# Performance work log

Hardware: AMD Instinct MI355X
Metric: run time of the kernel (lower is better)

Reference implementation:

```python
import jax, jax.numpy as jnp
import numpy as np

EPS = 1e-5

def _rmsnorm(x, eps=1e-6):
    # non-affine RMSNorm over last dim (BitNet SubLN-style pre-quant norm)
    return x * jax.lax.rsqrt(jnp.mean(x * x, axis=-1, keepdims=True) + eps)

def _act_quant(x):
    # per-token int8 absmax quantization
    scale = 127.0 / jnp.clip(jnp.max(jnp.abs(x), axis=-1, keepdims=True), EPS)
    return jnp.clip(jnp.round(x * scale), -128, 127) / scale

def _weight_quant(w):
    # per-tensor ternary (1.58-bit) quantization
    scale = 1.0 / jnp.clip(jnp.mean(jnp.abs(w)), EPS)
    return jnp.clip(jnp.round(w * scale), -1, 1) / scale

def _ste(a, q):
    # straight-through estimator: forward = q, backward grad flows to a
    return a + jax.lax.stop_gradient(q - a)

def _bitlinear(x, w):
    # x: [..., in_features], w: [out_features, in_features], no bias
    xn = _rmsnorm(x)
    xq = _ste(xn, _act_quant(xn))
    wq = _ste(w, _weight_quant(w))
    return jnp.einsum('bsd,hd->bsh', xq, wq)


def setup_inputs() -> dict:
    key = jax.random.key(0)
    k_x, k1, k2, k3 = jax.random.split(key, 4)
    B, S, D, H = 4, 4096, 2048, 5632  # hidden = 256*ceil(2048*8/3 / 256)
    return {
        'x': jax.random.normal(k_x, (B, S, D), dtype=jnp.float32),
        'w1': jax.random.normal(k1, (H, D), dtype=jnp.float32) * 0.02,
        'w2': jax.random.normal(k2, (H, D), dtype=jnp.float32) * 0.02,
        'w3': jax.random.normal(k3, (D, H), dtype=jnp.float32) * 0.02,
    }


def reference(x, w1, w2, w3):
    gate = jax.nn.silu(_bitlinear(x, w1))
    up = _bitlinear(x, w2)
    return _bitlinear(gate * up, w3)
```

## Files before the change

kernel.cpp:

```cpp
#include <hip/hip_runtime.h>

typedef int i32x4 __attribute__((ext_vector_type(4)));

static constexpr int M_TOK = 16384;
static constexpr int D_IN  = 2048;
static constexpr int H_FF  = 5632;
static constexpr int NW    = H_FF * D_IN;

__device__ __forceinline__ void async16(const void* g, void* l) {
    __builtin_amdgcn_global_load_lds((__attribute__((address_space(1))) void*)g,
                                     (__attribute__((address_space(3))) void*)l,
                                     16, 0, 0);
}

__device__ __forceinline__ void sbar() {
    asm volatile("" ::: "memory");
    __builtin_amdgcn_s_barrier();
    asm volatile("" ::: "memory");
}
#define WAIT_LGKM(n) { asm volatile("s_waitcnt lgkmcnt(" #n ")" ::: "memory"); \
                       __builtin_amdgcn_sched_barrier(0); }
#define WAIT_VM(n)   { asm volatile("s_waitcnt vmcnt(" #n ")" ::: "memory"); }

__global__ void absum_partial(const float4* __restrict__ w, int n4, double* __restrict__ part) {
    __shared__ double s[256];
    const int t = threadIdx.x;
    double acc = 0.0;
    for (int i = blockIdx.x * 256 + t; i < n4; i += gridDim.x * 256) {
        float4 v = w[i];
        acc += fabs((double)v.x) + fabs((double)v.y) + fabs((double)v.z) + fabs((double)v.w);
    }
    s[t] = acc;
    __syncthreads();
    for (int o = 128; o > 0; o >>= 1) {
        if (t < o) s[t] += s[t + o];
        __syncthreads();
    }
    if (t == 0) part[blockIdx.x] = s[0];
}

__global__ void finalize_scales(const double* __restrict__ parts, double* __restrict__ scales,
                                int nblocks, double inv_n) {
    const int t = threadIdx.x;
    if (t < 3) {
        const double* p = parts + t * nblocks;
        double s = 0.0;
        for (int i = 0; i < nblocks; ++i) s += p[i];
        double c = fmax(s * inv_n, 1e-5);
        scales[t * 2]     = 1.0 / c;
        scales[t * 2 + 1] = c;
    }
}

__global__ void quant_w_kernel(const float4* __restrict__ w, unsigned int* __restrict__ tw,
                               const double* __restrict__ scales, int idx, int n4) {
    const double s = scales[idx * 2];
    const int stride = gridDim.x * blockDim.x;
    for (int i = blockIdx.x * blockDim.x + threadIdx.x; i < n4; i += stride) {
        float4 v = w[i];
        int q0 = (int)fmin(fmax(rint((double)v.x * s), -1.0), 1.0);
        int q1 = (int)fmin(fmax(rint((double)v.y * s), -1.0), 1.0);
        int q2 = (int)fmin(fmax(rint((double)v.z * s), -1.0), 1.0);
        int q3 = (int)fmin(fmax(rint((double)v.w * s), -1.0), 1.0);
        tw[i] = (unsigned int)((q0 & 255) | ((q1 & 255) << 8) |
                               ((q2 & 255) << 16) | ((q3 & 255) << 24));
    }
}

__global__ void quant_x_kernel(const float* __restrict__ x, signed char* __restrict__ qx,
                               double* __restrict__ cx) {
    __shared__ double ssum[256];
    __shared__ float  smax[256];
    const int token = blockIdx.x;
    const int t = threadIdx.x;
    const float4* xr = (const float4*)(x + (size_t)token * D_IN);
    float4 v0 = xr[t];
    float4 v1 = xr[t + 256];
    double ss = (double)v0.x*v0.x + (double)v0.y*v0.y + (double)v0.z*v0.z + (double)v0.w*v0.w
              + (double)v1.x*v1.x + (double)v1.y*v1.y + (double)v1.z*v1.z + (double)v1.w*v1.w;
    float mx = fmaxf(fmaxf(fmaxf(fabsf(v0.x), fabsf(v0.y)), fmaxf(fabsf(v0.z), fabsf(v0.w))),
                     fmaxf(fmaxf(fabsf(v1.x), fabsf(v1.y)), fmaxf(fabsf(v1.z), fabsf(v1.w))));
    ssum[t] = ss; smax[t] = mx;
    __syncthreads();
    for (int o = 128; o > 0; o >>= 1) {
        if (t < o) { ssum[t] += ssum[t + o]; smax[t] = fmaxf(smax[t], smax[t + o]); }
        __syncthreads();
    }
    const double ms    = ssum[0] * (1.0 / (double)D_IN);
    const double r     = 1.0 / sqrt(ms + 1e-6);
    const double den   = fmax((double)smax[0] * r, 1e-5);
    const double scale = 127.0 / den;
    if (t == 0) cx[token] = den * (1.0 / 127.0);

    int q0 = (int)fmin(fmax(rint(((double)v0.x * r) * scale), -128.0), 127.0);
    int q1 = (int)fmin(fmax(rint(((double)v0.y * r) * scale), -128.0), 127.0);
    int q2 = (int)fmin(fmax(rint(((double)v0.z * r) * scale), -128.0), 127.0);
    int q3 = (int)fmin(fmax(rint(((double)v0.w * r) * scale), -128.0), 127.0);
    int q4 = (int)fmin(fmax(rint(((double)v1.x * r) * scale), -128.0), 127.0);
    int q5 = (int)fmin(fmax(rint(((double)v1.y * r) * scale), -128.0), 127.0);
    int q6 = (int)fmin(fmax(rint(((double)v1.z * r) * scale), -128.0), 127.0);
    int q7 = (int)fmin(fmax(rint(((double)v1.w * r) * scale), -128.0), 127.0);
    unsigned int* qr = (unsigned int*)(qx + (size_t)token * D_IN);
    qr[t]       = (unsigned int)((q0 & 255) | ((q1 & 255) << 8) | ((q2 & 255) << 16) | ((q3 & 255) << 24));
    qr[t + 256] = (unsigned int)((q4 & 255) | ((q5 & 255) << 8) | ((q6 & 255) << 16) | ((q7 & 255) << 24));
}

__global__ void quant_h_kernel(float* __restrict__ h, double* __restrict__ ch) {
    __shared__ double ssum[256];
    __shared__ float  smax[256];
    const int token = blockIdx.x;
    const int t = threadIdx.x;
    float* hr = h + (size_t)token * H_FF;
    const float2* h2 = (const float2*)hr;
    float2 vals[11];
    double ss = 0.0;
    float mx = 0.f;
#pragma unroll
    for (int k = 0; k < 11; ++k) {
        float2 v = h2[t + 256 * k];
        vals[k] = v;
        ss += (double)v.x * (double)v.x + (double)v.y * (double)v.y;
        mx = fmaxf(mx, fmaxf(fabsf(v.x), fabsf(v.y)));
    }
    ssum[t] = ss; smax[t] = mx;
    __syncthreads();
    for (int o = 128; o > 0; o >>= 1) {
        if (t < o) { ssum[t] += ssum[t + o]; smax[t] = fmaxf(smax[t], smax[t + o]); }
        __syncthreads();
    }
    const double ms    = ssum[0] * (1.0 / (double)H_FF);
    const double r     = 1.0 / sqrt(ms + 1e-6);
    const double den   = fmax((double)smax[0] * r, 1e-5);
    const double scale = 127.0 / den;
    if (t == 0) ch[token] = den * (1.0 / 127.0);
    unsigned short* qr = (unsigned short*)hr;
#pragma unroll
    for (int k = 0; k < 11; ++k) {
        int a = (int)fmin(fmax(rint(((double)vals[k].x * r) * scale), -128.0), 127.0);
        int b = (int)fmin(fmax(rint(((double)vals[k].y * r) * scale), -128.0), 127.0);
        qr[t + 256 * k] = (unsigned short)((a & 255) | ((b & 255) << 8));
    }
}


__global__ void __launch_bounds__(512, 4) gemm12_kernel(
    const signed char* __restrict__ qx,
    const signed char* __restrict__ tw1,
    const double* __restrict__ cx,
    const double* __restrict__ scales,
    float* __restrict__ h)
{
    __shared__ __attribute__((aligned(16))) signed char lds[2][24576];

    const int t = threadIdx.x;
    const int swz = (blockIdx.x & 7) * 704 + (blockIdx.x >> 3);
    const int bm  = swz / 88;
    const int bn  = swz % 88;

    const int srow = t >> 2;
    const int scol = (((t & 3) ^ ((t >> 3) & 3)) << 4);
    const signed char* gA = qx + (size_t)(bm * 256 + srow) * D_IN + scol;
    const size_t arstep = (size_t)128 * D_IN;
    const int brow = srow & 63;
    const signed char* gB = tw1 + (srow >= 64 ? (size_t)NW : (size_t)0)
                                + (size_t)(bn * 64 + brow) * D_IN + scol;
    const int l16 = t * 16;

    const int lane = t & 63;
    const int wv = t >> 6;
    const int wm = wv & 3;
    const int wn = wv >> 2;
    const int lm = lane & 15;
    const int kg = lane >> 4;
    const int koff  = ((kg ^ ((lm >> 1) & 3)) << 4);
    const int abase = (wm * 64 + lm) * 64 + koff;
    const int bbase = 16384 + (wn * 32 + lm) * 64 + koff;

    const i32x4 izero = {0, 0, 0, 0};
    i32x4 acc1[4][2], acc2[4][2];
#pragma unroll
    for (int i = 0; i < 4; ++i)
#pragma unroll
        for (int j = 0; j < 2; ++j) { acc1[i][j] = izero; acc2[i][j] = izero; }

    constexpr int NT = D_IN / 64;

#define STAGE12(buf, kt) { const int go = (kt) * 64;                         \
        async16(gA + go,          &lds[buf][l16]);                           \
        async16(gA + arstep + go, &lds[buf][8192 + l16]);                    \
        async16(gB + go,          &lds[buf][16384 + l16]); }

    STAGE12(0, 0);
    WAIT_VM(0); sbar();

    for (int kt = 0; kt < NT; ++kt) {
        const int cur = kt & 1;
        if (kt + 1 < NT) STAGE12(cur ^ 1, kt + 1);

        i32x4 a[4], b1[2], b2[2];
#pragma unroll
        for (int i = 0; i < 4; ++i) a[i] = *(const i32x4*)&lds[cur][abase + i * 1024];
#pragma unroll
        for (int j = 0; j < 2; ++j) b1[j] = *(const i32x4*)&lds[cur][bbase + j * 1024];
        __builtin_amdgcn_sched_barrier(0);
#pragma unroll
        for (int j = 0; j < 2; ++j) b2[j] = *(const i32x4*)&lds[cur][bbase + 4096 + j * 1024];

        WAIT_LGKM(2);
        __builtin_amdgcn_s_setprio(1);
#pragma unroll
        for (int i = 0; i < 4; ++i)
#pragma unroll
            for (int j = 0; j < 2; ++j)
                acc1[i][j] = __builtin_amdgcn_mfma_i32_16x16x64_i8(a[i], b1[j], acc1[i][j], 0, 0, 0);
        __builtin_amdgcn_s_setprio(0);
        WAIT_LGKM(0);
        __builtin_amdgcn_s_setprio(1);
#pragma unroll
        for (int i = 0; i < 4; ++i)
#pragma unroll
            for (int j = 0; j < 2; ++j)
                acc2[i][j] = __builtin_amdgcn_mfma_i32_16x16x64_i8(a[i], b2[j], acc2[i][j], 0, 0, 0);
        __builtin_amdgcn_s_setprio(0);

        WAIT_VM(0);
        sbar();
    }
#undef STAGE12

    const double cw1 = scales[1];
    const double cw2 = scales[3];
#pragma unroll
    for (int i = 0; i < 4; ++i) {
#pragma unroll
        for (int v = 0; v < 4; ++v) {
            const int row = bm * 256 + wm * 64 + i * 16 + kg * 4 + v;
            const double c  = cx[row];
            const double s1 = c * cw1, s2 = c * cw2;
            float* hp = h + (size_t)row * H_FF + bn * 64 + wn * 32 + lm;
#pragma unroll
            for (int j = 0; j < 2; ++j) {
                float g  = (float)((double)acc1[i][j][v] * s1);
                float u  = (float)((double)acc2[i][j][v] * s2);
                float sg = g / (1.0f + expf(-g));
                hp[j * 16] = sg * u;
            }
        }
    }
}

__global__ void __launch_bounds__(512, 4) gemm3_kernel(
    const signed char* __restrict__ qh,
    const signed char* __restrict__ tw3,
    const double* __restrict__ ch,
    const double* __restrict__ scales,
    float* __restrict__ out)
{
    __shared__ __attribute__((aligned(16))) signed char lds[2][24576];

    const int t = threadIdx.x;
    const int swz = (blockIdx.x & 7) * 128 + (blockIdx.x >> 3);
    const int bm  = swz >> 4;
    const int bn  = swz & 15;

    const int srow = t >> 2;
    const int scol = (((t & 3) ^ ((t >> 3) & 3)) << 4);
    const size_t qh_stride = (size_t)4 * H_FF;
    const signed char* gA = qh  + (size_t)(bm * 256 + srow) * qh_stride + scol;
    const signed char* gB = tw3 + (size_t)(bn * 128 + srow) * H_FF + scol;
    const size_t arstep = (size_t)128 * qh_stride;
    const int l16 = t * 16;

    const int lane = t & 63;
    const int wv = t >> 6;
    const int wm = wv & 3;
    const int wn = wv >> 2;
    const int lm = lane & 15;
    const int kg = lane >> 4;
    const int koff  = ((kg ^ ((lm >> 1) & 3)) << 4);
    const int abase = (wm * 64 + lm) * 64 + koff;
    const int bbase = 16384 + (wn * 64 + lm) * 64 + koff;

    const i32x4 izero = {0, 0, 0, 0};
    i32x4 acc[4][4];
#pragma unroll
    for (int i = 0; i < 4; ++i)
#pragma unroll
        for (int j = 0; j < 4; ++j) acc[i][j] = izero;

    constexpr int NT = H_FF / 64;

#define STAGE3(buf, kt) { const int go = (kt) * 64;                          \
        async16(gA + go,          &lds[buf][l16]);                           \
        async16(gA + arstep + go, &lds[buf][8192 + l16]);                    \
        async16(gB + go,          &lds[buf][16384 + l16]); }

    STAGE3(0, 0);
    WAIT_VM(0); sbar();

    for (int kt = 0; kt < NT; ++kt) {
        const int cur = kt & 1;
        if (kt + 1 < NT) STAGE3(cur ^ 1, kt + 1);

        i32x4 a[4], b[4];
#pragma unroll
        for (int i = 0; i < 4; ++i) a[i] = *(const i32x4*)&lds[cur][abase + i * 1024];
#pragma unroll
        for (int j = 0; j < 2; ++j) b[j] = *(const i32x4*)&lds[cur][bbase + j * 1024];
        __builtin_amdgcn_sched_barrier(0);
#pragma unroll
        for (int j = 2; j < 4; ++j) b[j] = *(const i32x4*)&lds[cur][bbase + j * 1024];

        WAIT_LGKM(2);
        __builtin_amdgcn_s_setprio(1);
#pragma unroll
        for (int i = 0; i < 4; ++i)
#pragma unroll
            for (int j = 0; j < 2; ++j)
                acc[i][j] = __builtin_amdgcn_mfma_i32_16x16x64_i8(a[i], b[j], acc[i][j], 0, 0, 0);
        __builtin_amdgcn_s_setprio(0);
        WAIT_LGKM(0);
        __builtin_amdgcn_s_setprio(1);
#pragma unroll
        for (int i = 0; i < 4; ++i)
#pragma unroll
            for (int j = 2; j < 4; ++j)
                acc[i][j] = __builtin_amdgcn_mfma_i32_16x16x64_i8(a[i], b[j], acc[i][j], 0, 0, 0);
        __builtin_amdgcn_s_setprio(0);

        WAIT_VM(0);
        sbar();
    }
#undef STAGE3

    const double cw3 = scales[5];
#pragma unroll
    for (int i = 0; i < 4; ++i) {
#pragma unroll
        for (int v = 0; v < 4; ++v) {
            const int row = bm * 256 + wm * 64 + i * 16 + kg * 4 + v;
            const double sc = ch[row] * cw3;
            float* op = out + (size_t)row * D_IN + bn * 128 + wn * 64 + lm;
#pragma unroll
            for (int j = 0; j < 4; ++j) op[j * 16] = (float)((double)acc[i][j][v] * sc);
        }
    }
}

extern "C" void kernel_launch(void* const* d_in, const int* in_sizes, int n_in,
                              void* d_out, int out_size, void* d_ws, size_t ws_size,
                              hipStream_t stream) {
    const float* x  = (const float*)d_in[0];
    const float* w1 = (const float*)d_in[1];
    const float* w2 = (const float*)d_in[2];
    const float* w3 = (const float*)d_in[3];

    char* ws = (char*)d_ws;
    double*      scales = (double*)(ws + 0);
    double*      parts  = (double*)(ws + 256);
    double*      cx     = (double*)(ws + 25088);
    double*      ch     = (double*)(ws + 156416);
    signed char* tw1    = (signed char*)(ws + 287744);
    signed char* tw2    = (signed char*)(ws + 11822080);
    signed char* tw3    = (signed char*)(ws + 23356416);
    float*       hb     = (float*)(ws + 34891520);
    signed char* qx     = (signed char*)(ws + 403990528);

    absum_partial<<<1024, 256, 0, stream>>>((const float4*)w1, NW / 4, parts);
    absum_partial<<<1024, 256, 0, stream>>>((const float4*)w2, NW / 4, parts + 1024);
    absum_partial<<<1024, 256, 0, stream>>>((const float4*)w3, NW / 4, parts + 2048);
    finalize_scales<<<1, 64, 0, stream>>>(parts, scales, 1024, 1.0 / (double)NW);
    quant_w_kernel<<<2048, 256, 0, stream>>>((const float4*)w1, (unsigned int*)tw1, scales, 0, NW / 4);
    quant_w_kernel<<<2048, 256, 0, stream>>>((const float4*)w2, (unsigned int*)tw2, scales, 1, NW / 4);
    quant_w_kernel<<<2048, 256, 0, stream>>>((const float4*)w3, (unsigned int*)tw3, scales, 2, NW / 4);
    quant_x_kernel<<<M_TOK, 256, 0, stream>>>(x, qx, cx);
    gemm12_kernel<<<5632, 512, 0, stream>>>(qx, tw1, cx, scales, hb);
    quant_h_kernel<<<M_TOK, 256, 0, stream>>>(hb, ch);
    gemm3_kernel<<<1024, 512, 0, stream>>>((const signed char*)hb, tw3, ch, scales, (float*)d_out);
}
```

Measured before the change: 1.095 ms.

## Load weight tiles directly to registers and triple-buffer activation LDS tiles

Both GEMM kernels now fetch the B (ternary weight) fragments straight from global memory into registers, double-buffered across iterations, instead of staging them through LDS. The A tiles move to a 3-deep LDS ring with a prefetch distance of two, and the block swizzle now walks M fastest so concurrent blocks share weight columns. This removes LDS traffic and bank pressure for B and gives the pipeline more load-latency slack. The cost is more VGPRs for the register-buffered B fragments, and less coalesced B global loads since each lane reads its own 16-byte slice.

```diff
diff --git a/kernel.cpp b/kernel.cpp
--- a/kernel.cpp
+++ b/kernel.cpp
@@ -6,6 +6,8 @@
 static constexpr int D_IN  = 2048;
 static constexpr int H_FF  = 5632;
 static constexpr int NW    = H_FF * D_IN;
+
+#define MFMA_I8 __builtin_amdgcn_mfma_i32_16x16x64_i8
 
 __device__ __forceinline__ void async16(const void* g, void* l) {
     __builtin_amdgcn_global_load_lds((__attribute__((address_space(1))) void*)g,
@@ -150,20 +152,17 @@
     const double* __restrict__ scales,
     float* __restrict__ h)
 {
-    __shared__ __attribute__((aligned(16))) signed char lds[2][24576];
+    __shared__ __attribute__((aligned(16))) signed char lds[3][16384];
 
     const int t = threadIdx.x;
     const int swz = (blockIdx.x & 7) * 704 + (blockIdx.x >> 3);
-    const int bm  = swz / 88;
-    const int bn  = swz % 88;
+    const int bm  = swz & 63;
+    const int bn  = swz >> 6;
 
     const int srow = t >> 2;
     const int scol = (((t & 3) ^ ((t >> 3) & 3)) << 4);
     const signed char* gA = qx + (size_t)(bm * 256 + srow) * D_IN + scol;
     const size_t arstep = (size_t)128 * D_IN;
-    const int brow = srow & 63;
-    const signed char* gB = tw1 + (srow >= 64 ? (size_t)NW : (size_t)0)
-                                + (size_t)(bn * 64 + brow) * D_IN + scol;
     const int l16 = t * 16;
 
     const int lane = t & 63;
@@ -174,7 +173,8 @@
     const int kg = lane >> 4;
     const int koff  = ((kg ^ ((lm >> 1) & 3)) << 4);
     const int abase = (wm * 64 + lm) * 64 + koff;
-    const int bbase = 16384 + (wn * 32 + lm) * 64 + koff;
+
+    const signed char* gB1 = tw1 + (size_t)(bn * 64 + wn * 32 + lm) * D_IN + kg * 16;
 
     const i32x4 izero = {0, 0, 0, 0};
     i32x4 acc1[4][2], acc2[4][2];
@@ -183,50 +183,53 @@
 #pragma unroll
         for (int j = 0; j < 2; ++j) { acc1[i][j] = izero; acc2[i][j] = izero; }
 
+    i32x4 bA[4], bB[4];
+
     constexpr int NT = D_IN / 64;
 
-#define STAGE12(buf, kt) { const int go = (kt) * 64;                         \
+#define STAGE_A12(buf, kt) { const int go = (kt) * 64;                       \
         async16(gA + go,          &lds[buf][l16]);                           \
-        async16(gA + arstep + go, &lds[buf][8192 + l16]);                    \
-        async16(gB + go,          &lds[buf][16384 + l16]); }
-
-    STAGE12(0, 0);
-    WAIT_VM(0); sbar();
-
-    for (int kt = 0; kt < NT; ++kt) {
-        const int cur = kt & 1;
-        if (kt + 1 < NT) STAGE12(cur ^ 1, kt + 1);
-
-        i32x4 a[4], b1[2], b2[2];
-#pragma unroll
-        for (int i = 0; i < 4; ++i) a[i] = *(const i32x4*)&lds[cur][abase + i * 1024];
-#pragma unroll
-        for (int j = 0; j < 2; ++j) b1[j] = *(const i32x4*)&lds[cur][bbase + j * 1024];
-        __builtin_amdgcn_sched_barrier(0);
-#pragma unroll
-        for (int j = 0; j < 2; ++j) b2[j] = *(const i32x4*)&lds[cur][bbase + 4096 + j * 1024];
-
-        WAIT_LGKM(2);
-        __builtin_amdgcn_s_setprio(1);
-#pragma unroll
-        for (int i = 0; i < 4; ++i)
-#pragma unroll
-            for (int j = 0; j < 2; ++j)
-                acc1[i][j] = __builtin_amdgcn_mfma_i32_16x16x64_i8(a[i], b1[j], acc1[i][j], 0, 0, 0);
-        __builtin_amdgcn_s_setprio(0);
-        WAIT_LGKM(0);
-        __builtin_amdgcn_s_setprio(1);
-#pragma unroll
-        for (int i = 0; i < 4; ++i)
-#pragma unroll
-            for (int j = 0; j < 2; ++j)
-                acc2[i][j] = __builtin_amdgcn_mfma_i32_16x16x64_i8(a[i], b2[j], acc2[i][j], 0, 0, 0);
-        __builtin_amdgcn_s_setprio(0);
-
-        WAIT_VM(0);
-        sbar();
-    }
-#undef STAGE12
+        async16(gA + arstep + go, &lds[buf][8192 + l16]); }
+#define LOADB12(R, kt) { const int go = (kt) * 64;                           \
+        R[0] = *(const i32x4*)(gB1 + go);                                    \
+        R[1] = *(const i32x4*)(gB1 + 16 * D_IN + go);                        \
+        R[2] = *(const i32x4*)(gB1 + NW + go);                               \
+        R[3] = *(const i32x4*)(gB1 + NW + 16 * D_IN + go); }
+#define TILE12(kt, RC, RN) {                                                 \
+        if ((kt) + 1 < NT) { LOADB12(RN, (kt) + 1); }                        \
+        __builtin_amdgcn_sched_barrier(0);                                   \
+        if ((kt) + 2 < NT) { STAGE_A12(((kt) + 2) % 3, (kt) + 2); }          \
+        __builtin_amdgcn_sched_barrier(0);                                   \
+        const int cb = (kt) % 3;                                             \
+        i32x4 a[4];                                                          \
+        _Pragma("unroll") for (int i = 0; i < 4; ++i)                        \
+            a[i] = *(const i32x4*)&lds[cb][abase + i * 1024];                \
+        WAIT_LGKM(0);                                                        \
+        __builtin_amdgcn_s_setprio(1);                                       \
+        _Pragma("unroll") for (int i = 0; i < 4; ++i) {                      \
+            acc1[i][0] = MFMA_I8(a[i], RC[0], acc1[i][0], 0, 0, 0);          \
+            acc1[i][1] = MFMA_I8(a[i], RC[1], acc1[i][1], 0, 0, 0);          \
+            acc2[i][0] = MFMA_I8(a[i], RC[2], acc2[i][0], 0, 0, 0);          \
+            acc2[i][1] = MFMA_I8(a[i], RC[3], acc2[i][1], 0, 0, 0); }        \
+        __builtin_amdgcn_s_setprio(0);                                       \
+        if ((kt) + 2 < NT) { WAIT_VM(2); } else { WAIT_VM(0); }              \
+        sbar(); }
+
+    STAGE_A12(0, 0);
+    __builtin_amdgcn_sched_barrier(0);
+    LOADB12(bA, 0);
+    __builtin_amdgcn_sched_barrier(0);
+    STAGE_A12(1, 1);
+    WAIT_VM(2);
+    sbar();
+
+    for (int kt = 0; kt < NT; kt += 2) {
+        TILE12(kt,     bA, bB);
+        TILE12(kt + 1, bB, bA);
+    }
+#undef STAGE_A12
+#undef LOADB12
+#undef TILE12
 
     const double cw1 = scales[1];
     const double cw2 = scales[3];
@@ -256,18 +259,17 @@
     const double* __restrict__ scales,
     float* __restrict__ out)
 {
-    __shared__ __attribute__((aligned(16))) signed char lds[2][24576];
+    __shared__ __attribute__((aligned(16))) signed char lds[3][16384];
 
     const int t = threadIdx.x;
     const int swz = (blockIdx.x & 7) * 128 + (blockIdx.x >> 3);
-    const int bm  = swz >> 4;
-    const int bn  = swz & 15;
+    const int bm  = swz & 63;
+    const int bn  = swz >> 6;
 
     const int srow = t >> 2;
     const int scol = (((t & 3) ^ ((t >> 3) & 3)) << 4);
     const size_t qh_stride = (size_t)4 * H_FF;
-    const signed char* gA = qh  + (size_t)(bm * 256 + srow) * qh_stride + scol;
-    const signed char* gB = tw3 + (size_t)(bn * 128 + srow) * H_FF + scol;
+    const signed char* gA = qh + (size_t)(bm * 256 + srow) * qh_stride + scol;
     const size_t arstep = (size_t)128 * qh_stride;
     const int l16 = t * 16;
 
@@ -279,7 +281,8 @@
     const int kg = lane >> 4;
     const int koff  = ((kg ^ ((lm >> 1) & 3)) << 4);
     const int abase = (wm * 64 + lm) * 64 + koff;
-    const int bbase = 16384 + (wn * 64 + lm) * 64 + koff;
+
+    const signed char* gB3 = tw3 + (size_t)(bn * 128 + wn * 64 + lm) * H_FF + kg * 16;
 
     const i32x4 izero = {0, 0, 0, 0};
     i32x4 acc[4][4];
@@ -288,50 +291,51 @@
 #pragma unroll
         for (int j = 0; j < 4; ++j) acc[i][j] = izero;
 
+    i32x4 bA[4], bB[4];
+
     constexpr int NT = H_FF / 64;
 
-#define STAGE3(buf, kt) { const int go = (kt) * 64;                          \
+#define STAGE_A3(buf, kt) { const int go = (kt) * 64;                        \
         async16(gA + go,          &lds[buf][l16]);                           \
-        async16(gA + arstep + go, &lds[buf][8192 + l16]);                    \
-        async16(gB + go,          &lds[buf][16384 + l16]); }
-
-    STAGE3(0, 0);
-    WAIT_VM(0); sbar();
-
-    for (int kt = 0; kt < NT; ++kt) {
-        const int cur = kt & 1;
-        if (kt + 1 < NT) STAGE3(cur ^ 1, kt + 1);
-
-        i32x4 a[4], b[4];
-#pragma unroll
-        for (int i = 0; i < 4; ++i) a[i] = *(const i32x4*)&lds[cur][abase + i * 1024];
-#pragma unroll
-        for (int j = 0; j < 2; ++j) b[j] = *(const i32x4*)&lds[cur][bbase + j * 1024];
-        __builtin_amdgcn_sched_barrier(0);
-#pragma unroll
-        for (int j = 2; j < 4; ++j) b[j] = *(const i32x4*)&lds[cur][bbase + j * 1024];
-
-        WAIT_LGKM(2);
-        __builtin_amdgcn_s_setprio(1);
-#pragma unroll
-        for (int i = 0; i < 4; ++i)
-#pragma unroll
-            for (int j = 0; j < 2; ++j)
-                acc[i][j] = __builtin_amdgcn_mfma_i32_16x16x64_i8(a[i], b[j], acc[i][j], 0, 0, 0);
-        __builtin_amdgcn_s_setprio(0);
-        WAIT_LGKM(0);
-        __builtin_amdgcn_s_setprio(1);
-#pragma unroll
-        for (int i = 0; i < 4; ++i)
-#pragma unroll
-            for (int j = 2; j < 4; ++j)
-                acc[i][j] = __builtin_amdgcn_mfma_i32_16x16x64_i8(a[i], b[j], acc[i][j], 0, 0, 0);
-        __builtin_amdgcn_s_setprio(0);
-
-        WAIT_VM(0);
-        sbar();
-    }
-#undef STAGE3
+        async16(gA + arstep + go, &lds[buf][8192 + l16]); }
+#define LOADB3(R, kt) { const int go = (kt) * 64;                            \
+        R[0] = *(const i32x4*)(gB3 + go);                                    \
+        R[1] = *(const i32x4*)(gB3 + 16 * H_FF + go);                        \
+        R[2] = *(const i32x4*)(gB3 + 32 * H_FF + go);                        \
+        R[3] = *(const i32x4*)(gB3 + 48 * H_FF + go); }
+#define TILE3(kt, RC, RN) {                                                  \
+        if ((kt) + 1 < NT) { LOADB3(RN, (kt) + 1); }                         \
+        __builtin_amdgcn_sched_barrier(0);                                   \
+        if ((kt) + 2 < NT) { STAGE_A3(((kt) + 2) % 3, (kt) + 2); }           \
+        __builtin_amdgcn_sched_barrier(0);                                   \
+        const int cb = (kt) % 3;                                             \
+        i32x4 a[4];                                                          \
+        _Pragma("unroll") for (int i = 0; i < 4; ++i)                        \
+            a[i] = *(const i32x4*)&lds[cb][abase + i * 1024];                \
+        WAIT_LGKM(0);                                                        \
+        __builtin_amdgcn_s_setprio(1);                                       \
+        _Pragma("unroll") for (int i = 0; i < 4; ++i)                        \
+        _Pragma("unroll") for (int j = 0; j < 4; ++j)                        \
+            acc[i][j] = MFMA_I8(a[i], RC[j], acc[i][j], 0, 0, 0);            \
+        __builtin_amdgcn_s_setprio(0);                                       \
+        if ((kt) + 2 < NT) { WAIT_VM(2); } else { WAIT_VM(0); }              \
+        sbar(); }
+
+    STAGE_A3(0, 0);
+    __builtin_amdgcn_sched_barrier(0);
+    LOADB3(bA, 0);
+    __builtin_amdgcn_sched_barrier(0);
+    STAGE_A3(1, 1);
+    WAIT_VM(2);
+    sbar();
+
+    for (int kt = 0; kt < NT; kt += 2) {
+        TILE3(kt,     bA, bB);
+        TILE3(kt + 1, bB, bA);
+    }
+#undef STAGE_A3
+#undef LOADB3
+#undef TILE3
 
     const double cw3 = scales[5];
 #pragma unroll
```

After: 1.725 ms. 57.5% more time.
